# Kernel optimization log

Measured on AMD Instinct MI355X. Metric: run time of the kernel, lower is better.

## Reference

```python
import jax, jax.numpy as jnp
import numpy as np

DIM = 96; NH = 3; HD = DIM // NH; SCALE = HD ** -0.5
WS = (7, 7, 7); N = WS[0] * WS[1] * WS[2]
SHIFT = (3, 3, 3)  # half window
NL = 2
GRID = (28, 28, 28)
B = 2


def _rel_index():
    wd, wh, ww = WS
    coords = np.stack(np.meshgrid(np.arange(wd), np.arange(wh), np.arange(ww), indexing='ij')).reshape(3, -1)
    rel = (coords[:, :, None] - coords[:, None, :]).transpose(1, 2, 0)  # [N,N,3]
    rel[..., 0] += wd - 1; rel[..., 1] += wh - 1; rel[..., 2] += ww - 1
    rel[..., 0] *= (2 * wh - 1) * (2 * ww - 1); rel[..., 1] *= (2 * ww - 1)
    return rel.sum(-1)  # [N,N]

REL_IDX = _rel_index()


def _window_partition(x):
    b, D, H, W, C = x.shape
    wd, wh, ww = WS
    x = x.reshape(b, D // wd, wd, H // wh, wh, W // ww, ww, C)
    x = x.transpose(0, 1, 3, 5, 2, 4, 6, 7)
    return x.reshape(-1, N, C)


def _window_reverse(win, b, D, H, W):
    wd, wh, ww = WS
    C = win.shape[-1]
    x = win.reshape(b, D // wd, H // wh, W // ww, wd, wh, ww, C)
    x = x.transpose(0, 1, 4, 2, 5, 3, 6, 7)
    return x.reshape(b, D, H, W, C)


def _compute_mask():
    # MONAI compute_mask for the shifted (SW-MSA) block
    D, H, W = GRID; wd, wh, ww = WS; sd, sh, sw = SHIFT
    img = np.zeros((1, D, H, W, 1), np.float32)
    cnt = 0
    for d in (slice(-wd), slice(-wd, -sd), slice(-sd, None)):
        for h in (slice(-wh), slice(-wh, -sh), slice(-sh, None)):
            for w in (slice(-ww), slice(-ww, -sw), slice(-sw, None)):
                img[:, d, h, w, :] = cnt; cnt += 1
    mw = img.reshape(1, D // wd, wd, H // wh, wh, W // ww, ww, 1)
    mw = mw.transpose(0, 1, 3, 5, 2, 4, 6, 7).reshape(-1, N)  # [nw, N]
    am = mw[:, None, :] - mw[:, :, None]
    return np.where(am != 0, np.float32(-100.0), np.float32(0.0))

MASK = jnp.asarray(_compute_mask())  # [nw, N, N]


def _ln(x, g, b):
    mu = x.mean(-1, keepdims=True)
    var = ((x - mu) ** 2).mean(-1, keepdims=True)
    return (x - mu) / jnp.sqrt(var + 1e-5) * g + b


def _block(x, p, shift, mask):
    b, D, H, W, C = x.shape
    h = _ln(x, p['n1g'], p['n1b'])
    if shift is not None:
        h = jnp.roll(h, (-shift[0], -shift[1], -shift[2]), axis=(1, 2, 3))
    xw = _window_partition(h)  # [b*nw, N, C]
    Bn = xw.shape[0]
    qkv = (xw @ p['qkvw'].T + p['qkvb']).reshape(Bn, N, 3, NH, HD).transpose(2, 0, 3, 1, 4)
    q, k, v = qkv[0] * SCALE, qkv[1], qkv[2]
    attn = jnp.einsum('bhnd,bhmd->bhnm', q, k)
    bias = p['rel'][REL_IDX.reshape(-1)].reshape(N, N, NH).transpose(2, 0, 1)
    attn = attn + bias[None]
    if mask is not None:
        nw = mask.shape[0]
        attn = (attn.reshape(Bn // nw, nw, NH, N, N) + mask[None, :, None]).reshape(Bn, NH, N, N)
    attn = jax.nn.softmax(attn, axis=-1)
    out = jnp.einsum('bhnm,bhmd->bhnd', attn, v).transpose(0, 2, 1, 3).reshape(Bn, N, C)
    out = out @ p['projw'].T + p['projb']
    h = _window_reverse(out, b, D, H, W)
    if shift is not None:
        h = jnp.roll(h, shift, axis=(1, 2, 3))
    x = x + h
    m = _ln(x, p['n2g'], p['n2b'])
    m = jax.nn.gelu(m @ p['fc1w'].T + p['fc1b'], approximate=False) @ p['fc2w'].T + p['fc2b']
    return x + m


def setup_inputs() -> dict:
    key = jax.random.key(0)
    ks = jax.random.split(key, 8)
    nbias = (2 * WS[0] - 1) * (2 * WS[1] - 1) * (2 * WS[2] - 1)
    return {
        'x': jax.random.normal(ks[0], (B,) + GRID + (DIM,), jnp.float32),
        'norm1_g': jnp.ones((NL, DIM), jnp.float32),
        'norm1_b': jnp.zeros((NL, DIM), jnp.float32),
        'qkv_w': jax.random.normal(ks[1], (NL, 3 * DIM, DIM), jnp.float32) * 0.02,
        'qkv_b': jnp.zeros((NL, 3 * DIM), jnp.float32),
        'rel_bias': jax.random.normal(ks[2], (NL, nbias, NH), jnp.float32) * 0.02,
        'proj_w': jax.random.normal(ks[3], (NL, DIM, DIM), jnp.float32) * 0.02,
        'proj_b': jnp.zeros((NL, DIM), jnp.float32),
        'norm2_g': jnp.ones((NL, DIM), jnp.float32),
        'norm2_b': jnp.zeros((NL, DIM), jnp.float32),
        'fc1_w': jax.random.normal(ks[4], (NL, 4 * DIM, DIM), jnp.float32) * 0.02,
        'fc1_b': jnp.zeros((NL, 4 * DIM), jnp.float32),
        'fc2_w': jax.random.normal(ks[5], (NL, DIM, 4 * DIM), jnp.float32) * 0.02,
        'fc2_b': jnp.zeros((NL, DIM), jnp.float32),
    }


def reference(x, norm1_g, norm1_b, qkv_w, qkv_b, rel_bias, proj_w, proj_b,
              norm2_g, norm2_b, fc1_w, fc1_b, fc2_w, fc2_b):
    for i in range(NL):
        p = dict(n1g=norm1_g[i], n1b=norm1_b[i], qkvw=qkv_w[i], qkvb=qkv_b[i],
                 rel=rel_bias[i], projw=proj_w[i], projb=proj_b[i],
                 n2g=norm2_g[i], n2b=norm2_b[i], fc1w=fc1_w[i], fc1b=fc1_b[i],
                 fc2w=fc2_w[i], fc2b=fc2_b[i])
        if i % 2 == 0:
            x = _block(x, p, None, None)  # W-MSA (mask is all-zero for shift=0)
        else:
            x = _block(x, p, SHIFT, MASK)  # SW-MSA
    return x
```

## Files before the change

kernel.cpp:

```cpp
#include <hip/hip_runtime.h>
#include <math.h>

#define DIM 96
#define NHD 3
#define HD 32
#define NWT 343
#define NWIN 128
#define TOK 43904
#define NBIAS 2197
#define SCALE 0.17677669529663687f
#define TPAD 352

typedef __attribute__((ext_vector_type(8))) short bf16x8;
typedef __attribute__((ext_vector_type(4))) float f32x4;

__device__ __forceinline__ unsigned short f2b(float f) {
    union { float f; unsigned int u; } x; x.f = f;
    unsigned int r = (x.u + 0x7fffu + ((x.u >> 16) & 1u)) >> 16;
    return (unsigned short)r;
}
__device__ __forceinline__ unsigned int pk2bf(float a, float b) {
    union { float f; unsigned int u; } x, y; x.f = a; y.f = b;
    return ((x.u + 0x8000u) >> 16) | ((y.u + 0x8000u) & 0xffff0000u);
}

__global__ void __launch_bounds__(256) k_cvt(const float* __restrict__ src,
                                             unsigned short* __restrict__ dst, int n) {
    int i = blockIdx.x * 256 + threadIdx.x;
    if (i < n) dst[i] = f2b(src[i]);
}

__global__ void __launch_bounds__(256) k_qkv(
        const float* __restrict__ x, const float* __restrict__ g1,
        const float* __restrict__ b1, const unsigned short* __restrict__ W,
        const float* __restrict__ bias, unsigned short* __restrict__ q,
        unsigned short* __restrict__ k, unsigned short* __restrict__ v, int shift) {
    __shared__ __align__(16) unsigned short lns[64][104];
    __shared__ __align__(16) unsigned short wbuf[96][104];
    int wid = threadIdx.x >> 6, lane = threadIdx.x & 63;
    int lm = lane & 15, q4 = lane >> 4;
    int m0 = blockIdx.x * 64 + wid * 16;
    int bwr[4], nnr[4];
    size_t rowoff[4];
    #pragma unroll
    for (int r = 0; r < 4; ++r) {
        int wtok = m0 + q4 * 4 + r;
        int bw = wtok / NWT, n = wtok % NWT;
        bwr[r] = bw; nnr[r] = n;
        int b = bw >> 6, win = bw & 63;
        int wdi = win >> 4, whi = (win >> 2) & 3, wwi = win & 3;
        int d = n / 49, h = (n / 7) % 7, w = n % 7;
        int sd = (wdi * 7 + d + shift) % 28;
        int sh = (whi * 7 + h + shift) % 28;
        int sw = (wwi * 7 + w + shift) % 28;
        rowoff[r] = (((size_t)(b * 28 + sd) * 28 + sh) * 28 + sw) * 96;
    }
    float val[6][4], g1v[6], b1v[6];
    #pragma unroll
    for (int c = 0; c < 6; ++c) {
        int ncol = c * 16 + lm;
        g1v[c] = g1[ncol]; b1v[c] = b1[ncol];
        #pragma unroll
        for (int r = 0; r < 4; ++r) val[c][r] = x[rowoff[r] + ncol];
    }
    #pragma unroll
    for (int r = 0; r < 4; ++r) {
        float s = 0.f, s2 = 0.f;
        #pragma unroll
        for (int c = 0; c < 6; ++c) { s += val[c][r]; s2 += val[c][r] * val[c][r]; }
        #pragma unroll
        for (int off = 8; off > 0; off >>= 1) {
            s  += __shfl_xor(s,  off, 64);
            s2 += __shfl_xor(s2, off, 64);
        }
        float mu = s * (1.0f / 96.0f);
        float rstd = rsqrtf(s2 * (1.0f / 96.0f) - mu * mu + 1e-5f);
        int row = wid * 16 + q4 * 4 + r;
        #pragma unroll
        for (int c = 0; c < 6; ++c)
            lns[row][c * 16 + lm] = f2b((val[c][r] - mu) * rstd * g1v[c] + b1v[c]);
    }
    __syncthreads();
    bf16x8 a1[3];
    #pragma unroll
    for (int ks = 0; ks < 3; ++ks)
        a1[ks] = *((const bf16x8*)&lns[wid * 16 + lm][ks * 32 + q4 * 8]);
    for (int ch = 0; ch < 3; ++ch) {
        __syncthreads();
        const uint4* src = (const uint4*)(W + ch * 96 * 96);
        for (int s = threadIdx.x; s < 1152; s += 256) {
            int row = s / 12, seg = s % 12;
            *((uint4*)&wbuf[row][seg * 8]) = src[s];
        }
        __syncthreads();
        f32x4 acc[6];
        #pragma unroll
        for (int c = 0; c < 6; ++c) acc[c] = (f32x4){0.f, 0.f, 0.f, 0.f};
        #pragma unroll
        for (int ks = 0; ks < 3; ++ks) {
            #pragma unroll
            for (int c = 0; c < 6; ++c) {
                bf16x8 b = *((const bf16x8*)&wbuf[c * 16 + lm][ks * 32 + q4 * 8]);
                acc[c] = __builtin_amdgcn_mfma_f32_16x16x32_bf16(a1[ks], b, acc[c], 0, 0, 0);
            }
        }
        #pragma unroll
        for (int c = 0; c < 6; ++c) {
            int col = c * 16 + lm;
            int head = col >> 5, hd = col & 31;
            float bb = bias[ch * 96 + col];
            #pragma unroll
            for (int r = 0; r < 4; ++r) {
                int wh = bwr[r] * NHD + head;
                float vv = acc[c][r] + bb;
                if (ch == 0)
                    q[(size_t)wh * (TPAD * 32) + nnr[r] * 32 + hd] = f2b(vv * SCALE);
                else if (ch == 1)
                    k[(size_t)wh * (TPAD * 32) + nnr[r] * 32 + hd] = f2b(vv);
                else
                    v[(size_t)wh * (32 * TPAD) + hd * TPAD + nnr[r]] = f2b(vv);
            }
        }
    }
}

__global__ void __launch_bounds__(256) k_attn(
        const unsigned short* __restrict__ q, const unsigned short* __restrict__ k,
        const unsigned short* __restrict__ vT, const float* __restrict__ rel,
        unsigned short* __restrict__ o, int shifted) {
    __shared__ float relh[NBIAS];
    __shared__ int   jinfo[NWT];
    __shared__ __align__(16) unsigned short vts[32 * 360];
    __shared__ __align__(16) unsigned short pbuf[4][16 * 40];
    __shared__ float dnm[4][16];
    int wh = blockIdx.x >> 1, half = blockIdx.x & 1;
    int bw = wh / NHD, head = wh % NHD;
    for (int i = threadIdx.x; i < NBIAS; i += 256) relh[i] = rel[i * NHD + head];
    const unsigned int* vsrc = (const unsigned int*)(vT + (size_t)wh * 32 * TPAD);
    unsigned int* vdst = (unsigned int*)vts;
    for (int i = threadIdx.x; i < 32 * 176; i += 256) {
        int row = i / 176, cc = i - row * 176;
        vdst[row * 180 + cc] = vsrc[i];
    }
    int win = bw & 63;
    int wdi = win >> 4, whi = (win >> 2) & 3, wwi = win & 3;
    for (int i = threadIdx.x; i < NWT; i += 256) {
        int d = i / 49, h = (i / 7) % 7, w = i % 7;
        int gd = wdi * 7 + d, gh = whi * 7 + h, gw = wwi * 7 + w;
        int rd = (gd < 21) ? 0 : ((gd < 25) ? 1 : 2);
        int rh = (gh < 21) ? 0 : ((gh < 25) ? 1 : 2);
        int rw = (gw < 21) ? 0 : ((gw < 25) ? 1 : 2);
        jinfo[i] = (d * 169 + h * 13 + w) | ((rd * 9 + rh * 3 + rw) << 16);
    }
    __syncthreads();
    int wid = threadIdx.x >> 6, lane = threadIdx.x & 63;
    int lm = lane & 15, q4 = lane >> 4;
    const unsigned short* qbase = q + (size_t)wh * TPAD * 32;
    const unsigned short* kbase = k + (size_t)wh * TPAD * 32;
    unsigned short* pb = pbuf[wid];
    for (int qtl = wid; qtl < 11; qtl += 4) {
        int qt = half * 11 + qtl;
        int qtok = qt * 16 + lm;
        bf16x8 qf = *((const bf16x8*)(qbase + qtok * 32 + q4 * 8));
        int jq = jinfo[min(qtok, NWT - 1)];
        int jqc = (jq & 0xffff) + 1098;
        int rq = jq >> 16;
        f32x4 acc0 = (f32x4){0.f, 0.f, 0.f, 0.f};
        f32x4 acc1 = (f32x4){0.f, 0.f, 0.f, 0.f};
        float denom = 0.f;
        for (int pr = 0; pr < 11; ++pr) {
            int kb0 = pr * 32;
            bf16x8 kf0 = *((const bf16x8*)(kbase + (kb0 + lm) * 32 + q4 * 8));
            bf16x8 kf1 = *((const bf16x8*)(kbase + (kb0 + 16 + lm) * 32 + q4 * 8));
            f32x4 z = (f32x4){0.f, 0.f, 0.f, 0.f};
            f32x4 s0 = __builtin_amdgcn_mfma_f32_16x16x32_bf16(kf0, qf, z, 0, 0, 0);
            f32x4 s1 = __builtin_amdgcn_mfma_f32_16x16x32_bf16(kf1, qf, z, 0, 0, 0);
            float p[8];
            #pragma unroll
            for (int t = 0; t < 2; ++t) {
                #pragma unroll
                for (int r = 0; r < 4; ++r) {
                    int key = kb0 + t * 16 + q4 * 4 + r;
                    int jk = jinfo[min(key, NWT - 1)];
                    float s = (t ? s1[r] : s0[r]) + relh[jqc - (jk & 0xffff)];
                    if (shifted && ((jk >> 16) != rq)) s -= 100.0f;
                    float pv = __expf(s);
                    pv = (key < NWT) ? pv : 0.0f;
                    p[t * 4 + r] = pv;
                    denom += pv;
                }
            }
            #pragma unroll
            for (int t = 0; t < 2; ++t) {
                *((unsigned int*)(pb + lm * 40 + t * 16 + q4 * 4)) =
                    pk2bf(p[t * 4 + 0], p[t * 4 + 1]);
                *((unsigned int*)(pb + lm * 40 + t * 16 + q4 * 4 + 2)) =
                    pk2bf(p[t * 4 + 2], p[t * 4 + 3]);
            }
            bf16x8 pf = *((const bf16x8*)(pb + lm * 40 + q4 * 8));
            bf16x8 v0 = *((const bf16x8*)(vts + lm * 360 + kb0 + q4 * 8));
            bf16x8 v1 = *((const bf16x8*)(vts + (16 + lm) * 360 + kb0 + q4 * 8));
            acc0 = __builtin_amdgcn_mfma_f32_16x16x32_bf16(pf, v0, acc0, 0, 0, 0);
            acc1 = __builtin_amdgcn_mfma_f32_16x16x32_bf16(pf, v1, acc1, 0, 0, 0);
        }
        denom += __shfl_xor(denom, 16, 64);
        denom += __shfl_xor(denom, 32, 64);
        if (lane < 16) dnm[wid][lm] = denom;
        #pragma unroll
        for (int r = 0; r < 4; ++r) {
            int qrow = qt * 16 + q4 * 4 + r;
            if (qrow < NWT) {
                float inv = 1.0f / dnm[wid][q4 * 4 + r];
                unsigned short* op = o + (size_t)(bw * NWT + qrow) * DIM + head * HD;
                op[lm]      = f2b(acc0[r] * inv);
                op[16 + lm] = f2b(acc1[r] * inv);
            }
        }
    }
}

__global__ void __launch_bounds__(256) k_proj(
        const unsigned short* __restrict__ ao, const unsigned short* __restrict__ W,
        const float* __restrict__ bias, const float* __restrict__ xin,
        float* __restrict__ xout, unsigned short* __restrict__ lnb,
        const float* __restrict__ g2, const float* __restrict__ b2, int shift) {
    __shared__ __align__(16) unsigned short wbuf[96][104];
    for (int s = threadIdx.x; s < 1152; s += 256) {
        int row = s / 12, seg = s % 12;
        *((uint4*)&wbuf[row][seg * 8]) = ((const uint4*)W)[s];
    }
    int wid = threadIdx.x >> 6, lane = threadIdx.x & 63;
    int m0 = blockIdx.x * 64 + wid * 16;
    int lm = lane & 15, q4 = lane >> 4;
    const unsigned short* arow = ao + (size_t)(m0 + lm) * 96;
    bf16x8 a1[3];
    #pragma unroll
    for (int ks = 0; ks < 3; ++ks)
        a1[ks] = *((const bf16x8*)(arow + ks * 32 + q4 * 8));
    __syncthreads();
    f32x4 acc[6];
    #pragma unroll
    for (int c = 0; c < 6; ++c) acc[c] = (f32x4){0.f, 0.f, 0.f, 0.f};
    #pragma unroll
    for (int ks = 0; ks < 3; ++ks) {
        #pragma unroll
        for (int c = 0; c < 6; ++c) {
            bf16x8 b = *((const bf16x8*)&wbuf[c * 16 + lm][ks * 32 + q4 * 8]);
            acc[c] = __builtin_amdgcn_mfma_f32_16x16x32_bf16(a1[ks], b, acc[c], 0, 0, 0);
        }
    }
    size_t rowoff[4];
    #pragma unroll
    for (int r = 0; r < 4; ++r) {
        int wtok = m0 + q4 * 4 + r;
        int bw = wtok / NWT, n = wtok % NWT;
        int b = bw >> 6, win = bw & 63;
        int wdi = win >> 4, whi = (win >> 2) & 3, wwi = win & 3;
        int d = n / 49, h = (n / 7) % 7, w = n % 7;
        int sd = (wdi * 7 + d + shift) % 28;
        int sh = (whi * 7 + h + shift) % 28;
        int sw = (wwi * 7 + w + shift) % 28;
        rowoff[r] = (((size_t)(b * 28 + sd) * 28 + sh) * 28 + sw) * 96;
    }
    float val[6][4];
    float g2v[6], b2v[6];
    #pragma unroll
    for (int c = 0; c < 6; ++c) {
        int n = c * 16 + lm;
        float bb = bias[n];
        g2v[c] = g2[n]; b2v[c] = b2[n];
        #pragma unroll
        for (int r = 0; r < 4; ++r) {
            size_t off = rowoff[r] + n;
            float y = xin[off] + acc[c][r] + bb;
            val[c][r] = y;
            xout[off] = y;
        }
    }
    #pragma unroll
    for (int r = 0; r < 4; ++r) {
        float s = 0.f, s2 = 0.f;
        #pragma unroll
        for (int c = 0; c < 6; ++c) { s += val[c][r]; s2 += val[c][r] * val[c][r]; }
        #pragma unroll
        for (int off = 8; off > 0; off >>= 1) {
            s  += __shfl_xor(s,  off, 64);
            s2 += __shfl_xor(s2, off, 64);
        }
        float mu = s * (1.0f / 96.0f);
        float rstd = rsqrtf(s2 * (1.0f / 96.0f) - mu * mu + 1e-5f);
        #pragma unroll
        for (int c = 0; c < 6; ++c) {
            lnb[rowoff[r] + c * 16 + lm] =
                f2b((val[c][r] - mu) * rstd * g2v[c] + b2v[c]);
        }
    }
}

__global__ void __launch_bounds__(256) k_mlp(
        const unsigned short* __restrict__ lnb, const float* __restrict__ xmid,
        float* __restrict__ xout,
        const unsigned short* __restrict__ w1, const float* __restrict__ bb1,
        const unsigned short* __restrict__ w2, const float* __restrict__ bb2) {
    __shared__ __align__(16) unsigned short w1s[64][104];
    __shared__ __align__(16) unsigned short w2s[96][76];
    __shared__ __align__(16) unsigned short hid[4][16][76];
    int wid = threadIdx.x >> 6, lane = threadIdx.x & 63;
    int lm = lane & 15, q4 = lane >> 4;
    int m0w = blockIdx.x * 64 + wid * 16;
    bf16x8 a1[3];
    const unsigned short* arow = lnb + (size_t)(m0w + lm) * 96;
    #pragma unroll
    for (int ks = 0; ks < 3; ++ks)
        a1[ks] = *((const bf16x8*)(arow + ks * 32 + q4 * 8));
    f32x4 acc2[6];
    #pragma unroll
    for (int c = 0; c < 6; ++c) acc2[c] = (f32x4){0.f, 0.f, 0.f, 0.f};
    unsigned short* hw_ = &hid[wid][0][0];
    for (int ch = 0; ch < 6; ++ch) {
        __syncthreads();
        const uint4* src1 = (const uint4*)(w1 + ch * 64 * 96);
        #pragma unroll
        for (int t = 0; t < 3; ++t) {
            int s = threadIdx.x + t * 256;
            int row = s / 12, seg = s % 12;
            *((uint4*)&w1s[row][seg * 8]) = src1[s];
        }
        #pragma unroll
        for (int t = 0; t < 3; ++t) {
            int s = threadIdx.x + t * 256;
            int row = s >> 3, seg = s & 7;
            *((uint4*)&w2s[row][seg * 8]) =
                *((const uint4*)(w2 + row * 384 + ch * 64 + seg * 8));
        }
        __syncthreads();
        f32x4 acc1[4];
        #pragma unroll
        for (int t = 0; t < 4; ++t) acc1[t] = (f32x4){0.f, 0.f, 0.f, 0.f};
        #pragma unroll
        for (int ks = 0; ks < 3; ++ks) {
            #pragma unroll
            for (int t = 0; t < 4; ++t) {
                bf16x8 b = *((const bf16x8*)&w1s[t * 16 + lm][ks * 32 + q4 * 8]);
                acc1[t] = __builtin_amdgcn_mfma_f32_16x16x32_bf16(a1[ks], b, acc1[t], 0, 0, 0);
            }
        }
        #pragma unroll
        for (int t = 0; t < 4; ++t) {
            float bb = bb1[ch * 64 + t * 16 + lm];
            #pragma unroll
            for (int r = 0; r < 4; ++r) {
                float v2 = acc1[t][r] + bb;
                float ge = 0.5f * v2 * (1.0f + erff(v2 * 0.70710678118654752f));
                hw_[(q4 * 4 + r) * 76 + t * 16 + lm] = f2b(ge);
            }
        }
        #pragma unroll
        for (int ks2 = 0; ks2 < 2; ++ks2) {
            bf16x8 a = *((const bf16x8*)(hw_ + lm * 76 + ks2 * 32 + q4 * 8));
            #pragma unroll
            for (int c = 0; c < 6; ++c) {
                bf16x8 b = *((const bf16x8*)&w2s[c * 16 + lm][ks2 * 32 + q4 * 8]);
                acc2[c] = __builtin_amdgcn_mfma_f32_16x16x32_bf16(a, b, acc2[c], 0, 0, 0);
            }
        }
    }
    #pragma unroll
    for (int c = 0; c < 6; ++c) {
        int n = c * 16 + lm;
        float bb = bb2[n];
        #pragma unroll
        for (int r = 0; r < 4; ++r) {
            size_t off = (size_t)(m0w + q4 * 4 + r) * 96 + n;
            xout[off] = xmid[off] + acc2[c][r] + bb;
        }
    }
}

extern "C" void kernel_launch(void* const* d_in, const int* in_sizes, int n_in,
                              void* d_out, int out_size, void* d_ws, size_t ws_size,
                              hipStream_t stream) {
    const float* x     = (const float*)d_in[0];
    const float* n1g   = (const float*)d_in[1];
    const float* n1b   = (const float*)d_in[2];
    const float* qkvw  = (const float*)d_in[3];
    const float* qkvb  = (const float*)d_in[4];
    const float* relb  = (const float*)d_in[5];
    const float* projw = (const float*)d_in[6];
    const float* projb = (const float*)d_in[7];
    const float* n2g   = (const float*)d_in[8];
    const float* n2b   = (const float*)d_in[9];
    const float* fc1w  = (const float*)d_in[10];
    const float* fc1b  = (const float*)d_in[11];
    const float* fc2w  = (const float*)d_in[12];
    const float* fc2b  = (const float*)d_in[13];
    float* out = (float*)d_out;

    const size_t NEL = (size_t)TOK * DIM;
    const size_t QKN = (size_t)NWIN * NHD * TPAD * 32;
    float* buf_x = (float*)d_ws;
    unsigned short* hbuf = (unsigned short*)(buf_x + NEL);
    unsigned short* lnb  = hbuf + NEL;
    unsigned short* bq   = lnb + NEL;
    unsigned short* bk   = bq + QKN;
    unsigned short* bv   = bk + QKN;
    unsigned short* wts  = bv + QKN;
    unsigned short* wq  = wts;
    unsigned short* wp  = wq + 2 * 27648;
    unsigned short* w1  = wp + 2 * 9216;
    unsigned short* w2  = w1 + 2 * 36864;

    k_cvt<<<(2 * 27648 + 255) / 256, 256, 0, stream>>>(qkvw, wq, 2 * 27648);
    k_cvt<<<(2 * 9216  + 255) / 256, 256, 0, stream>>>(projw, wp, 2 * 9216);
    k_cvt<<<(2 * 36864 + 255) / 256, 256, 0, stream>>>(fc1w, w1, 2 * 36864);
    k_cvt<<<(2 * 36864 + 255) / 256, 256, 0, stream>>>(fc2w, w2, 2 * 36864);

    for (int L = 0; L < 2; ++L) {
        int shift = (L == 0) ? 0 : 3;
        const float* xin_l = (L == 0) ? x : buf_x;
        float* xfin = (L == 0) ? buf_x : out;

        k_qkv<<<TOK / 64, 256, 0, stream>>>(xin_l, n1g + L * 96, n1b + L * 96,
                                            wq + L * 27648, qkvb + L * 288,
                                            bq, bk, bv, shift);
        k_attn<<<NWIN * NHD * 2, 256, 0, stream>>>(bq, bk, bv, relb + L * NBIAS * NHD, hbuf,
                                                   shift ? 1 : 0);
        k_proj<<<TOK / 64, 256, 0, stream>>>(hbuf, wp + L * 9216, projb + L * 96,
                                             xin_l, buf_x, lnb,
                                             n2g + L * 96, n2b + L * 96, shift);
        k_mlp<<<TOK / 64, 256, 0, stream>>>(lnb, buf_x, xfin,
                                            w1 + L * 36864, fc1b + L * 384,
                                            w2 + L * 36864, fc2b + L * 96);
    }
}
```

Measured before the change: 295.5 us.

## Fuse proj and MLP kernels, dual query tiles per wave, merge weight conversions

Merges the projection+LN2 kernel with the MLP kernel so the residual and normalized activations stay in registers and LDS instead of round-tripping through global memory. The attention kernel now splits each window-head across three blocks, and each wave handles two query tiles that share the same K and V fragments. The four weight-conversion launches are combined into one. The trade-off is more registers and LDS per block in the fused kernel, which may lower occupancy. Some waves in the last attention block do no work.

Result: faster. 269.7 us (-8.7%).

```diff
diff --git a/kernel.cpp b/kernel.cpp
--- a/kernel.cpp
+++ b/kernel.cpp
@@ -24,10 +24,18 @@
     return ((x.u + 0x8000u) >> 16) | ((y.u + 0x8000u) & 0xffff0000u);
 }
 
-__global__ void __launch_bounds__(256) k_cvt(const float* __restrict__ src,
-                                             unsigned short* __restrict__ dst, int n) {
+__global__ void __launch_bounds__(256) k_cvt4(
+        const float* __restrict__ s0, const float* __restrict__ s1,
+        const float* __restrict__ s2, const float* __restrict__ s3,
+        unsigned short* __restrict__ dst) {
     int i = blockIdx.x * 256 + threadIdx.x;
-    if (i < n) dst[i] = f2b(src[i]);
+    if (i >= 221184) return;
+    const float* src; int off;
+    if (i < 55296)       { src = s0; off = i; }
+    else if (i < 73728)  { src = s1; off = i - 55296; }
+    else if (i < 147456) { src = s2; off = i - 73728; }
+    else                 { src = s3; off = i - 147456; }
+    dst[i] = f2b(src[off]);
 }
 
 __global__ void __launch_bounds__(256) k_qkv(
@@ -131,9 +139,9 @@
     __shared__ float relh[NBIAS];
     __shared__ int   jinfo[NWT];
     __shared__ __align__(16) unsigned short vts[32 * 360];
-    __shared__ __align__(16) unsigned short pbuf[4][16 * 40];
-    __shared__ float dnm[4][16];
-    int wh = blockIdx.x >> 1, half = blockIdx.x & 1;
+    __shared__ __align__(16) unsigned short pbuf[4][2][16 * 40];
+    __shared__ float dnm[4][2][16];
+    int wh = blockIdx.x / 3, third = blockIdx.x % 3;
     int bw = wh / NHD, head = wh % NHD;
     for (int i = threadIdx.x; i < NBIAS; i += 256) relh[i] = rel[i * NHD + head];
     const unsigned int* vsrc = (const unsigned int*)(vT + (size_t)wh * 32 * TPAD);
@@ -155,83 +163,114 @@
     __syncthreads();
     int wid = threadIdx.x >> 6, lane = threadIdx.x & 63;
     int lm = lane & 15, q4 = lane >> 4;
+    int tb = third * 8 + wid * 2;
+    if (tb > 21) return;
+    bool dual = (tb + 1 <= 21);
+    int qtA = tb, qtB = dual ? tb + 1 : tb;
     const unsigned short* qbase = q + (size_t)wh * TPAD * 32;
     const unsigned short* kbase = k + (size_t)wh * TPAD * 32;
-    unsigned short* pb = pbuf[wid];
-    for (int qtl = wid; qtl < 11; qtl += 4) {
-        int qt = half * 11 + qtl;
-        int qtok = qt * 16 + lm;
-        bf16x8 qf = *((const bf16x8*)(qbase + qtok * 32 + q4 * 8));
-        int jq = jinfo[min(qtok, NWT - 1)];
-        int jqc = (jq & 0xffff) + 1098;
-        int rq = jq >> 16;
-        f32x4 acc0 = (f32x4){0.f, 0.f, 0.f, 0.f};
-        f32x4 acc1 = (f32x4){0.f, 0.f, 0.f, 0.f};
-        float denom = 0.f;
-        for (int pr = 0; pr < 11; ++pr) {
-            int kb0 = pr * 32;
-            bf16x8 kf0 = *((const bf16x8*)(kbase + (kb0 + lm) * 32 + q4 * 8));
-            bf16x8 kf1 = *((const bf16x8*)(kbase + (kb0 + 16 + lm) * 32 + q4 * 8));
-            f32x4 z = (f32x4){0.f, 0.f, 0.f, 0.f};
-            f32x4 s0 = __builtin_amdgcn_mfma_f32_16x16x32_bf16(kf0, qf, z, 0, 0, 0);
-            f32x4 s1 = __builtin_amdgcn_mfma_f32_16x16x32_bf16(kf1, qf, z, 0, 0, 0);
-            float p[8];
-            #pragma unroll
-            for (int t = 0; t < 2; ++t) {
-                #pragma unroll
-                for (int r = 0; r < 4; ++r) {
-                    int key = kb0 + t * 16 + q4 * 4 + r;
-                    int jk = jinfo[min(key, NWT - 1)];
-                    float s = (t ? s1[r] : s0[r]) + relh[jqc - (jk & 0xffff)];
-                    if (shifted && ((jk >> 16) != rq)) s -= 100.0f;
-                    float pv = __expf(s);
-                    pv = (key < NWT) ? pv : 0.0f;
-                    p[t * 4 + r] = pv;
-                    denom += pv;
-                }
-            }
-            #pragma unroll
-            for (int t = 0; t < 2; ++t) {
-                *((unsigned int*)(pb + lm * 40 + t * 16 + q4 * 4)) =
-                    pk2bf(p[t * 4 + 0], p[t * 4 + 1]);
-                *((unsigned int*)(pb + lm * 40 + t * 16 + q4 * 4 + 2)) =
-                    pk2bf(p[t * 4 + 2], p[t * 4 + 3]);
-            }
-            bf16x8 pf = *((const bf16x8*)(pb + lm * 40 + q4 * 8));
-            bf16x8 v0 = *((const bf16x8*)(vts + lm * 360 + kb0 + q4 * 8));
-            bf16x8 v1 = *((const bf16x8*)(vts + (16 + lm) * 360 + kb0 + q4 * 8));
-            acc0 = __builtin_amdgcn_mfma_f32_16x16x32_bf16(pf, v0, acc0, 0, 0, 0);
-            acc1 = __builtin_amdgcn_mfma_f32_16x16x32_bf16(pf, v1, acc1, 0, 0, 0);
-        }
-        denom += __shfl_xor(denom, 16, 64);
-        denom += __shfl_xor(denom, 32, 64);
-        if (lane < 16) dnm[wid][lm] = denom;
+    int qtokA = qtA * 16 + lm, qtokB = qtB * 16 + lm;
+    bf16x8 qfA = *((const bf16x8*)(qbase + qtokA * 32 + q4 * 8));
+    bf16x8 qfB = *((const bf16x8*)(qbase + qtokB * 32 + q4 * 8));
+    int jqA = jinfo[min(qtokA, NWT - 1)], jqB = jinfo[min(qtokB, NWT - 1)];
+    int jqcA = (jqA & 0xffff) + 1098, rqA = jqA >> 16;
+    int jqcB = (jqB & 0xffff) + 1098, rqB = jqB >> 16;
+    f32x4 aA0 = (f32x4){0.f,0.f,0.f,0.f}, aA1 = aA0, aB0 = aA0, aB1 = aA0;
+    float dA = 0.f, dB = 0.f;
+    unsigned short* pbA = pbuf[wid][0];
+    unsigned short* pbB = pbuf[wid][1];
+    for (int pr = 0; pr < 11; ++pr) {
+        int kb0 = pr * 32;
+        bf16x8 kf0 = *((const bf16x8*)(kbase + (kb0 + lm) * 32 + q4 * 8));
+        bf16x8 kf1 = *((const bf16x8*)(kbase + (kb0 + 16 + lm) * 32 + q4 * 8));
+        f32x4 z = (f32x4){0.f, 0.f, 0.f, 0.f};
+        f32x4 sA0 = __builtin_amdgcn_mfma_f32_16x16x32_bf16(kf0, qfA, z, 0, 0, 0);
+        f32x4 sA1 = __builtin_amdgcn_mfma_f32_16x16x32_bf16(kf1, qfA, z, 0, 0, 0);
+        f32x4 sB0 = __builtin_amdgcn_mfma_f32_16x16x32_bf16(kf0, qfB, z, 0, 0, 0);
+        f32x4 sB1 = __builtin_amdgcn_mfma_f32_16x16x32_bf16(kf1, qfB, z, 0, 0, 0);
+        float pA[8], pB[8];
+        #pragma unroll
+        for (int t = 0; t < 2; ++t) {
+            #pragma unroll
+            for (int r = 0; r < 4; ++r) {
+                int key = kb0 + t * 16 + q4 * 4 + r;
+                int jk = jinfo[min(key, NWT - 1)];
+                int jkc = jk & 0xffff, rk = jk >> 16;
+                bool pad = key >= NWT;
+                float sA_ = (t ? sA1[r] : sA0[r]) + relh[jqcA - jkc];
+                if (shifted && (rk != rqA)) sA_ -= 100.0f;
+                float pvA = pad ? 0.0f : __expf(sA_);
+                dA += pvA; pA[t * 4 + r] = pvA;
+                float sB_ = (t ? sB1[r] : sB0[r]) + relh[jqcB - jkc];
+                if (shifted && (rk != rqB)) sB_ -= 100.0f;
+                float pvB = pad ? 0.0f : __expf(sB_);
+                dB += pvB; pB[t * 4 + r] = pvB;
+            }
+        }
+        #pragma unroll
+        for (int t = 0; t < 2; ++t) {
+            *((unsigned int*)(pbA + lm * 40 + t * 16 + q4 * 4)) =
+                pk2bf(pA[t * 4 + 0], pA[t * 4 + 1]);
+            *((unsigned int*)(pbA + lm * 40 + t * 16 + q4 * 4 + 2)) =
+                pk2bf(pA[t * 4 + 2], pA[t * 4 + 3]);
+            *((unsigned int*)(pbB + lm * 40 + t * 16 + q4 * 4)) =
+                pk2bf(pB[t * 4 + 0], pB[t * 4 + 1]);
+            *((unsigned int*)(pbB + lm * 40 + t * 16 + q4 * 4 + 2)) =
+                pk2bf(pB[t * 4 + 2], pB[t * 4 + 3]);
+        }
+        bf16x8 pfA = *((const bf16x8*)(pbA + lm * 40 + q4 * 8));
+        bf16x8 pfB = *((const bf16x8*)(pbB + lm * 40 + q4 * 8));
+        bf16x8 v0 = *((const bf16x8*)(vts + lm * 360 + kb0 + q4 * 8));
+        bf16x8 v1 = *((const bf16x8*)(vts + (16 + lm) * 360 + kb0 + q4 * 8));
+        aA0 = __builtin_amdgcn_mfma_f32_16x16x32_bf16(pfA, v0, aA0, 0, 0, 0);
+        aA1 = __builtin_amdgcn_mfma_f32_16x16x32_bf16(pfA, v1, aA1, 0, 0, 0);
+        aB0 = __builtin_amdgcn_mfma_f32_16x16x32_bf16(pfB, v0, aB0, 0, 0, 0);
+        aB1 = __builtin_amdgcn_mfma_f32_16x16x32_bf16(pfB, v1, aB1, 0, 0, 0);
+    }
+    dA += __shfl_xor(dA, 16, 64); dA += __shfl_xor(dA, 32, 64);
+    dB += __shfl_xor(dB, 16, 64); dB += __shfl_xor(dB, 32, 64);
+    if (lane < 16) { dnm[wid][0][lm] = dA; dnm[wid][1][lm] = dB; }
+    #pragma unroll
+    for (int r = 0; r < 4; ++r) {
+        int qrowA = qtA * 16 + q4 * 4 + r;
+        if (qrowA < NWT) {
+            float inv = 1.0f / dnm[wid][0][q4 * 4 + r];
+            unsigned short* op = o + (size_t)(bw * NWT + qrowA) * DIM + head * HD;
+            op[lm]      = f2b(aA0[r] * inv);
+            op[16 + lm] = f2b(aA1[r] * inv);
+        }
+    }
+    if (dual) {
         #pragma unroll
         for (int r = 0; r < 4; ++r) {
-            int qrow = qt * 16 + q4 * 4 + r;
-            if (qrow < NWT) {
-                float inv = 1.0f / dnm[wid][q4 * 4 + r];
-                unsigned short* op = o + (size_t)(bw * NWT + qrow) * DIM + head * HD;
-                op[lm]      = f2b(acc0[r] * inv);
-                op[16 + lm] = f2b(acc1[r] * inv);
-            }
-        }
-    }
-}
-
-__global__ void __launch_bounds__(256) k_proj(
-        const unsigned short* __restrict__ ao, const unsigned short* __restrict__ W,
-        const float* __restrict__ bias, const float* __restrict__ xin,
-        float* __restrict__ xout, unsigned short* __restrict__ lnb,
-        const float* __restrict__ g2, const float* __restrict__ b2, int shift) {
-    __shared__ __align__(16) unsigned short wbuf[96][104];
+            int qrowB = qtB * 16 + q4 * 4 + r;
+            if (qrowB < NWT) {
+                float inv = 1.0f / dnm[wid][1][q4 * 4 + r];
+                unsigned short* op = o + (size_t)(bw * NWT + qrowB) * DIM + head * HD;
+                op[lm]      = f2b(aB0[r] * inv);
+                op[16 + lm] = f2b(aB1[r] * inv);
+            }
+        }
+    }
+}
+
+__global__ void __launch_bounds__(256) k_pm(
+        const unsigned short* __restrict__ ao, const unsigned short* __restrict__ Wp,
+        const float* __restrict__ pbias, const float* __restrict__ xin,
+        float* __restrict__ xout,
+        const float* __restrict__ g2, const float* __restrict__ b2,
+        const unsigned short* __restrict__ w1, const float* __restrict__ bb1,
+        const unsigned short* __restrict__ w2, const float* __restrict__ bb2,
+        int shift) {
+    __shared__ __align__(16) unsigned short lns[64][104];
+    __shared__ __align__(16) unsigned short big[18816];
+    int wid = threadIdx.x >> 6, lane = threadIdx.x & 63;
+    int lm = lane & 15, q4 = lane >> 4;
+    int m0 = blockIdx.x * 64 + wid * 16;
     for (int s = threadIdx.x; s < 1152; s += 256) {
         int row = s / 12, seg = s % 12;
-        *((uint4*)&wbuf[row][seg * 8]) = ((const uint4*)W)[s];
-    }
-    int wid = threadIdx.x >> 6, lane = threadIdx.x & 63;
-    int m0 = blockIdx.x * 64 + wid * 16;
-    int lm = lane & 15, q4 = lane >> 4;
+        *((uint4*)&big[row * 104 + seg * 8]) = ((const uint4*)Wp)[s];
+    }
     const unsigned short* arow = ao + (size_t)(m0 + lm) * 96;
     bf16x8 a1[3];
     #pragma unroll
@@ -245,7 +284,7 @@
     for (int ks = 0; ks < 3; ++ks) {
         #pragma unroll
         for (int c = 0; c < 6; ++c) {
-            bf16x8 b = *((const bf16x8*)&wbuf[c * 16 + lm][ks * 32 + q4 * 8]);
+            bf16x8 b = *((const bf16x8*)&big[(c * 16 + lm) * 104 + ks * 32 + q4 * 8]);
             acc[c] = __builtin_amdgcn_mfma_f32_16x16x32_bf16(a1[ks], b, acc[c], 0, 0, 0);
         }
     }
@@ -262,20 +301,15 @@
         int sw = (wwi * 7 + w + shift) % 28;
         rowoff[r] = (((size_t)(b * 28 + sd) * 28 + sh) * 28 + sw) * 96;
     }
-    float val[6][4];
-    float g2v[6], b2v[6];
+    float val[6][4], g2v[6], b2v[6];
     #pragma unroll
     for (int c = 0; c < 6; ++c) {
         int n = c * 16 + lm;
-        float bb = bias[n];
+        float bb = pbias[n];
         g2v[c] = g2[n]; b2v[c] = b2[n];
         #pragma unroll
-        for (int r = 0; r < 4; ++r) {
-            size_t off = rowoff[r] + n;
-            float y = xin[off] + acc[c][r] + bb;
-            val[c][r] = y;
-            xout[off] = y;
-        }
+        for (int r = 0; r < 4; ++r)
+            val[c][r] = xin[rowoff[r] + n] + acc[c][r] + bb;
     }
     #pragma unroll
     for (int r = 0; r < 4; ++r) {
@@ -289,34 +323,19 @@
         }
         float mu = s * (1.0f / 96.0f);
         float rstd = rsqrtf(s2 * (1.0f / 96.0f) - mu * mu + 1e-5f);
-        #pragma unroll
-        for (int c = 0; c < 6; ++c) {
-            lnb[rowoff[r] + c * 16 + lm] =
-                f2b((val[c][r] - mu) * rstd * g2v[c] + b2v[c]);
-        }
-    }
-}
-
-__global__ void __launch_bounds__(256) k_mlp(
-        const unsigned short* __restrict__ lnb, const float* __restrict__ xmid,
-        float* __restrict__ xout,
-        const unsigned short* __restrict__ w1, const float* __restrict__ bb1,
-        const unsigned short* __restrict__ w2, const float* __restrict__ bb2) {
-    __shared__ __align__(16) unsigned short w1s[64][104];
-    __shared__ __align__(16) unsigned short w2s[96][76];
-    __shared__ __align__(16) unsigned short hid[4][16][76];
-    int wid = threadIdx.x >> 6, lane = threadIdx.x & 63;
-    int lm = lane & 15, q4 = lane >> 4;
-    int m0w = blockIdx.x * 64 + wid * 16;
-    bf16x8 a1[3];
-    const unsigned short* arow = lnb + (size_t)(m0w + lm) * 96;
+        int row = wid * 16 + q4 * 4 + r;
+        #pragma unroll
+        for (int c = 0; c < 6; ++c)
+            lns[row][c * 16 + lm] = f2b((val[c][r] - mu) * rstd * g2v[c] + b2v[c]);
+    }
+    bf16x8 am[3];
     #pragma unroll
     for (int ks = 0; ks < 3; ++ks)
-        a1[ks] = *((const bf16x8*)(arow + ks * 32 + q4 * 8));
+        am[ks] = *((const bf16x8*)&lns[wid * 16 + lm][ks * 32 + q4 * 8]);
     f32x4 acc2[6];
     #pragma unroll
     for (int c = 0; c < 6; ++c) acc2[c] = (f32x4){0.f, 0.f, 0.f, 0.f};
-    unsigned short* hw_ = &hid[wid][0][0];
+    unsigned short* hid_ = &big[13952 + wid * 1216];
     for (int ch = 0; ch < 6; ++ch) {
         __syncthreads();
         const uint4* src1 = (const uint4*)(w1 + ch * 64 * 96);
@@ -324,13 +343,13 @@
         for (int t = 0; t < 3; ++t) {
             int s = threadIdx.x + t * 256;
             int row = s / 12, seg = s % 12;
-            *((uint4*)&w1s[row][seg * 8]) = src1[s];
+            *((uint4*)&big[row * 104 + seg * 8]) = src1[s];
         }
         #pragma unroll
         for (int t = 0; t < 3; ++t) {
             int s = threadIdx.x + t * 256;
             int row = s >> 3, seg = s & 7;
-            *((uint4*)&w2s[row][seg * 8]) =
+            *((uint4*)&big[6656 + row * 76 + seg * 8]) =
                 *((const uint4*)(w2 + row * 384 + ch * 64 + seg * 8));
         }
         __syncthreads();
@@ -341,8 +360,8 @@
         for (int ks = 0; ks < 3; ++ks) {
             #pragma unroll
             for (int t = 0; t < 4; ++t) {
-                bf16x8 b = *((const bf16x8*)&w1s[t * 16 + lm][ks * 32 + q4 * 8]);
-                acc1[t] = __builtin_amdgcn_mfma_f32_16x16x32_bf16(a1[ks], b, acc1[t], 0, 0, 0);
+                bf16x8 b = *((const bf16x8*)&big[(t * 16 + lm) * 104 + ks * 32 + q4 * 8]);
+                acc1[t] = __builtin_amdgcn_mfma_f32_16x16x32_bf16(am[ks], b, acc1[t], 0, 0, 0);
             }
         }
         #pragma unroll
@@ -352,15 +371,15 @@
             for (int r = 0; r < 4; ++r) {
                 float v2 = acc1[t][r] + bb;
                 float ge = 0.5f * v2 * (1.0f + erff(v2 * 0.70710678118654752f));
-                hw_[(q4 * 4 + r) * 76 + t * 16 + lm] = f2b(ge);
+                hid_[(q4 * 4 + r) * 76 + t * 16 + lm] = f2b(ge);
             }
         }
         #pragma unroll
         for (int ks2 = 0; ks2 < 2; ++ks2) {
-            bf16x8 a = *((const bf16x8*)(hw_ + lm * 76 + ks2 * 32 + q4 * 8));
+            bf16x8 a = *((const bf16x8*)(hid_ + lm * 76 + ks2 * 32 + q4 * 8));
             #pragma unroll
             for (int c = 0; c < 6; ++c) {
-                bf16x8 b = *((const bf16x8*)&w2s[c * 16 + lm][ks2 * 32 + q4 * 8]);
+                bf16x8 b = *((const bf16x8*)&big[6656 + (c * 16 + lm) * 76 + ks2 * 32 + q4 * 8]);
                 acc2[c] = __builtin_amdgcn_mfma_f32_16x16x32_bf16(a, b, acc2[c], 0, 0, 0);
             }
         }
@@ -370,10 +389,8 @@
         int n = c * 16 + lm;
         float bb = bb2[n];
         #pragma unroll
-        for (int r = 0; r < 4; ++r) {
-            size_t off = (size_t)(m0w + q4 * 4 + r) * 96 + n;
-            xout[off] = xmid[off] + acc2[c][r] + bb;
-        }
+        for (int r = 0; r < 4; ++r)
+            xout[rowoff[r] + n] = val[c][r] + acc2[c][r] + bb;
     }
 }
 
@@ -400,8 +417,7 @@
     const size_t QKN = (size_t)NWIN * NHD * TPAD * 32;
     float* buf_x = (float*)d_ws;
     unsigned short* hbuf = (unsigned short*)(buf_x + NEL);
-    unsigned short* lnb  = hbuf + NEL;
-    unsigned short* bq   = lnb + NEL;
+    unsigned short* bq   = hbuf + NEL;
     unsigned short* bk   = bq + QKN;
     unsigned short* bv   = bk + QKN;
     unsigned short* wts  = bv + QKN;
@@ -410,10 +426,7 @@
     unsigned short* w1  = wp + 2 * 9216;
     unsigned short* w2  = w1 + 2 * 36864;
 
-    k_cvt<<<(2 * 27648 + 255) / 256, 256, 0, stream>>>(qkvw, wq, 2 * 27648);
-    k_cvt<<<(2 * 9216  + 255) / 256, 256, 0, stream>>>(projw, wp, 2 * 9216);
-    k_cvt<<<(2 * 36864 + 255) / 256, 256, 0, stream>>>(fc1w, w1, 2 * 36864);
-    k_cvt<<<(2 * 36864 + 255) / 256, 256, 0, stream>>>(fc2w, w2, 2 * 36864);
+    k_cvt4<<<(221184 + 255) / 256, 256, 0, stream>>>(qkvw, projw, fc1w, fc2w, wts);
 
     for (int L = 0; L < 2; ++L) {
         int shift = (L == 0) ? 0 : 3;
@@ -423,13 +436,12 @@
         k_qkv<<<TOK / 64, 256, 0, stream>>>(xin_l, n1g + L * 96, n1b + L * 96,
                                             wq + L * 27648, qkvb + L * 288,
                                             bq, bk, bv, shift);
-        k_attn<<<NWIN * NHD * 2, 256, 0, stream>>>(bq, bk, bv, relb + L * NBIAS * NHD, hbuf,
+        k_attn<<<NWIN * NHD * 3, 256, 0, stream>>>(bq, bk, bv, relb + L * NBIAS * NHD, hbuf,
                                                    shift ? 1 : 0);
-        k_proj<<<TOK / 64, 256, 0, stream>>>(hbuf, wp + L * 9216, projb + L * 96,
-                                             xin_l, buf_x, lnb,
-                                             n2g + L * 96, n2b + L * 96, shift);
-        k_mlp<<<TOK / 64, 256, 0, stream>>>(lnb, buf_x, xfin,
-                                            w1 + L * 36864, fc1b + L * 384,
-                                            w2 + L * 36864, fc2b + L * 96);
-    }
-}
+        k_pm<<<TOK / 64, 256, 0, stream>>>(hbuf, wp + L * 9216, projb + L * 96,
+                                           xin_l, xfin,
+                                           n2g + L * 96, n2b + L * 96,
+                                           w1 + L * 36864, fc1b + L * 384,
+                                           w2 + L * 36864, fc2b + L * 96, shift);
+    }
+}
```
